# Kernel tuning notes

Hardware: AMD Instinct MI355X
Metric: run time of the kernel (lower is better)

The kernel has to match this reference:

```python
import jax, jax.numpy as jnp
import numpy as np

B, T, D_IN, H = 2048, 240, 180, 90


def setup_inputs() -> dict:
    key = jax.random.key(0)
    k1, k2, k3, k4, k5 = jax.random.split(key, 5)
    s = 1.0 / np.sqrt(H)  # torch LSTMCell init scale
    return {
        "x": jax.random.normal(k1, (B, 3, 60, 240), dtype=jnp.float32),
        "W_ih": jax.random.uniform(k2, (4 * H, D_IN), dtype=jnp.float32, minval=-s, maxval=s),
        "W_hh": jax.random.uniform(k3, (4 * H, H), dtype=jnp.float32, minval=-s, maxval=s),
        "b_ih": jax.random.uniform(k4, (4 * H,), dtype=jnp.float32, minval=-s, maxval=s),
        "b_hh": jax.random.uniform(k5, (4 * H,), dtype=jnp.float32, minval=-s, maxval=s),
    }


def reference(x, W_ih, W_hh, b_ih, b_hh):
    # (B, 3, 60, 240) -> (B, 240, 3, 60) -> (B, 240, 180)
    b = x.shape[0]
    xt = jnp.transpose(x, (0, 3, 1, 2)).reshape(b, T, D_IN)
    # NOTE: the torch module calls LSTMCell without carrying state, so h0=c0=0
    # at EVERY timestep; the W_hh contribution is identically zero and all
    # timesteps are independent -> one batched GEMM over (B*T).
    gates = jnp.einsum("bti,gi->btg", xt, W_ih) + b_ih + b_hh  # (B, T, 4H)
    i_g, f_g, g_g, o_g = jnp.split(gates, 4, axis=-1)  # torch gate order i,f,g,o
    c = jax.nn.sigmoid(i_g) * jnp.tanh(g_g)  # f_g * c_prev = 0
    h = jax.nn.sigmoid(o_g) * jnp.tanh(c)
    return jax.nn.sigmoid(h)  # (B, T, H)
```

## Files before the change

### kernel.cpp

```cpp
#include <hip/hip_runtime.h>


#define B_SZ 2048
#define T_SZ 240
#define K_SZ 180
#define H_SZ 90
#define KP   192
#define TB   80
#define NP   3
#define NTT  5

#define WS_B_OFF 110592

typedef __bf16 bf16x8 __attribute__((ext_vector_type(8)));
typedef __bf16 bf16x4 __attribute__((ext_vector_type(4)));
typedef float  f32x4  __attribute__((ext_vector_type(4)));

__device__ __forceinline__ float sigmoidf_(float x) {
    return __builtin_amdgcn_rcpf(1.0f + __expf(-x));
}
__device__ __forceinline__ float tanhf_(float x) {
    return 1.0f - 2.0f * __builtin_amdgcn_rcpf(__expf(2.0f * x) + 1.0f);
}

__device__ __forceinline__ int skey(int t) {
    return (2 * (t + (t >> 4))) & 14;
}
__device__ __forceinline__ int sgran(int g, int t) {
    return (g & ~15) | ((g ^ skey(t)) & 15);
}

__global__ __launch_bounds__(384) void prepack_kernel(
    const float* __restrict__ W_ih,
    const float* __restrict__ b_ih,
    const float* __restrict__ b_hh,
    void* __restrict__ ws)
{
    __bf16* wp = (__bf16*)ws;
    float*  bp = (float*)((char*)ws + WS_B_OFF);
    const int gb[3] = {0, 180, 270};

    const int bid = blockIdx.x;
    const int tid = threadIdx.x;
    if (bid < 18) {
        const int g  = bid / 6;
        const int ks = bid % 6;
        const int w  = tid >> 6;
        const int l  = tid & 63;
        const int q  = l >> 4;
        const int n  = l & 15;
        const int h  = w * 16 + n;
        bf16x8 f;
        #pragma unroll
        for (int j = 0; j < 8; ++j) {
            int k = ks * 32 + q * 8 + j;
            float v = (h < H_SZ && k < K_SZ) ? W_ih[(size_t)(gb[g] + h) * K_SZ + k] : 0.0f;
            f[j] = (__bf16)v;
        }
        *(bf16x8*)(wp + (size_t)(((g * 6 + ks) * 6 + w) * 64 + l) * 8) = f;
    } else {
        if (tid < 288) {
            int g = tid / 96, hh = tid % 96;
            bp[g * 96 + hh] = (hh < H_SZ) ? (b_ih[gb[g] + hh] + b_hh[gb[g] + hh]) : 0.0f;
        }
    }
}

__global__ __launch_bounds__(384, 3) void lstm_fused_kernel(
    const float* __restrict__ x,
    const void*  __restrict__ ws,
    float* __restrict__ out)
{
    __shared__ __align__(16) __bf16 aBuf[TB * KP];

    const int bid  = blockIdx.x;
    const int b    = bid / NP;
    const int part = bid - b * NP;
    const int t0   = part * TB;

    const int tid  = threadIdx.x;
    const int wave = tid >> 6;
    const int lane = tid & 63;
    const int q    = lane >> 4;
    const int n    = lane & 15;
    const int h    = wave * 16 + n;
    const bool hv  = (h < H_SZ);

    const float* xb = x + (size_t)b * (K_SZ * T_SZ) + t0;

    if (tid < TB * 3) {
        int t  = tid / 3;
        int gz = 45 + (tid - (tid / 3) * 3);
        *(unsigned long long*)(aBuf + t * KP + sgran(gz, t) * 4) = 0ull;
    }

    #pragma unroll
    for (int p = 0; p < 3; ++p) {
        int u = tid + p * 384;
        if (p < 2 || u < 900) {
            int k4 = u / 20;
            int t4 = u - k4 * 20;
            const float* src = xb + (k4 * 4) * T_SZ + t4 * 4;
            f32x4 r0 = *(const f32x4*)(src);
            f32x4 r1 = *(const f32x4*)(src + T_SZ);
            f32x4 r2 = *(const f32x4*)(src + 2 * T_SZ);
            f32x4 r3 = *(const f32x4*)(src + 3 * T_SZ);
            #pragma unroll
            for (int j = 0; j < 4; ++j) {
                int t = t4 * 4 + j;
                bf16x4 w;
                w[0] = (__bf16)r0[j]; w[1] = (__bf16)r1[j];
                w[2] = (__bf16)r2[j]; w[3] = (__bf16)r3[j];
                *(bf16x4*)(aBuf + t * KP + sgran(k4, t) * 4) = w;
            }
        }
    }

    const bf16x8* wp = (const bf16x8*)ws;
    bf16x8 bfrag[3][6];
    #pragma unroll
    for (int g = 0; g < 3; ++g)
        #pragma unroll
        for (int ks = 0; ks < 6; ++ks)
            bfrag[g][ks] = wp[((g * 6 + ks) * 6 + wave) * 64 + lane];

    const float* bp = (const float*)((const char*)ws + WS_B_OFF);
    const float bias_i = bp[0 * 96 + h];
    const float bias_g = bp[1 * 96 + h];
    const float bias_o = bp[2 * 96 + h];
    float* ob = out + (size_t)b * (T_SZ * H_SZ) + (size_t)t0 * H_SZ;

    __syncthreads();

    #pragma unroll
    for (int tt = 0; tt < NTT; ++tt) {
        f32x4 acc0 = {0.f, 0.f, 0.f, 0.f};
        f32x4 acc1 = {0.f, 0.f, 0.f, 0.f};
        f32x4 acc2 = {0.f, 0.f, 0.f, 0.f};
        const int t = tt * 16 + n;
        #pragma unroll
        for (int ks = 0; ks < 6; ++ks) {
            int g = ks * 8 + 2 * q;
            bf16x8 a = *(const bf16x8*)(aBuf + t * KP + sgran(g, t) * 4);
            acc0 = __builtin_amdgcn_mfma_f32_16x16x32_bf16(a, bfrag[0][ks], acc0, 0, 0, 0);
            acc1 = __builtin_amdgcn_mfma_f32_16x16x32_bf16(a, bfrag[1][ks], acc1, 0, 0, 0);
            acc2 = __builtin_amdgcn_mfma_f32_16x16x32_bf16(a, bfrag[2][ks], acc2, 0, 0, 0);
        }
        if (hv) {
            const int tg = tt * 16 + q * 4;
            #pragma unroll
            for (int e = 0; e < 4; ++e) {
                float gi = acc0[e] + bias_i;
                float gg = acc1[e] + bias_g;
                float go = acc2[e] + bias_o;
                float cc = sigmoidf_(gi) * tanhf_(gg);
                float hh = sigmoidf_(go) * tanhf_(cc);
                ob[(size_t)(tg + e) * H_SZ + h] = sigmoidf_(hh);
            }
        }
        if (tt + 1 < NTT) __builtin_amdgcn_s_barrier();
    }
}

extern "C" void kernel_launch(void* const* d_in, const int* in_sizes, int n_in,
                              void* d_out, int out_size, void* d_ws, size_t ws_size,
                              hipStream_t stream) {
    const float* x    = (const float*)d_in[0];
    const float* W_ih = (const float*)d_in[1];
    const float* b_ih = (const float*)d_in[3];
    const float* b_hh = (const float*)d_in[4];
    float* out = (float*)d_out;

    prepack_kernel<<<dim3(19), dim3(384), 0, stream>>>(W_ih, b_ih, b_hh, d_ws);
    lstm_fused_kernel<<<dim3(B_SZ * NP), dim3(384), 0, stream>>>(x, d_ws, out);
}
```

Baseline: 554.5 us.

## Make LSTM kernel persistent with double-buffered LDS prefetch of input tiles

Replaces the one-block-per-tile grid with 512 persistent blocks, each handling 12 consecutive (batch, time-part) tiles. The global loads for the next tile are issued into registers before the MFMA and epilogue work on the current tile, then written to a second LDS buffer, so load latency overlaps with compute. This also amortises the per-block weight-fragment and bias loads across tiles. In exchange it doubles LDS use, raises register pressure from the prefetch registers, and leaves fewer blocks in the grid, which may lower occupancy and load balance.

```diff
diff --git a/kernel.cpp b/kernel.cpp
--- a/kernel.cpp
+++ b/kernel.cpp
@@ -7,8 +7,10 @@
 #define H_SZ 90
 #define KP   192
 #define TB   80
-#define NP   3
 #define NTT  5
+#define BPB  4
+#define NPARTS 12
+#define NBLK 512
 
 #define WS_B_OFF 110592
 
@@ -71,12 +73,7 @@
     const void*  __restrict__ ws,
     float* __restrict__ out)
 {
-    __shared__ __align__(16) __bf16 aBuf[TB * KP];
-
-    const int bid  = blockIdx.x;
-    const int b    = bid / NP;
-    const int part = bid - b * NP;
-    const int t0   = part * TB;
+    __shared__ __align__(16) __bf16 aBuf[2][TB * KP];
 
     const int tid  = threadIdx.x;
     const int wave = tid >> 6;
@@ -86,36 +83,6 @@
     const int h    = wave * 16 + n;
     const bool hv  = (h < H_SZ);
 
-    const float* xb = x + (size_t)b * (K_SZ * T_SZ) + t0;
-
-    if (tid < TB * 3) {
-        int t  = tid / 3;
-        int gz = 45 + (tid - (tid / 3) * 3);
-        *(unsigned long long*)(aBuf + t * KP + sgran(gz, t) * 4) = 0ull;
-    }
-
-    #pragma unroll
-    for (int p = 0; p < 3; ++p) {
-        int u = tid + p * 384;
-        if (p < 2 || u < 900) {
-            int k4 = u / 20;
-            int t4 = u - k4 * 20;
-            const float* src = xb + (k4 * 4) * T_SZ + t4 * 4;
-            f32x4 r0 = *(const f32x4*)(src);
-            f32x4 r1 = *(const f32x4*)(src + T_SZ);
-            f32x4 r2 = *(const f32x4*)(src + 2 * T_SZ);
-            f32x4 r3 = *(const f32x4*)(src + 3 * T_SZ);
-            #pragma unroll
-            for (int j = 0; j < 4; ++j) {
-                int t = t4 * 4 + j;
-                bf16x4 w;
-                w[0] = (__bf16)r0[j]; w[1] = (__bf16)r1[j];
-                w[2] = (__bf16)r2[j]; w[3] = (__bf16)r3[j];
-                *(bf16x4*)(aBuf + t * KP + sgran(k4, t) * 4) = w;
-            }
-        }
-    }
-
     const bf16x8* wp = (const bf16x8*)ws;
     bf16x8 bfrag[3][6];
     #pragma unroll
@@ -128,38 +95,111 @@
     const float bias_i = bp[0 * 96 + h];
     const float bias_g = bp[1 * 96 + h];
     const float bias_o = bp[2 * 96 + h];
-    float* ob = out + (size_t)b * (T_SZ * H_SZ) + (size_t)t0 * H_SZ;
-
+
+    if (tid < TB * 3) {
+        int t  = tid / 3;
+        int gz = 45 + (tid - (tid / 3) * 3);
+        *(unsigned long long*)(aBuf[0] + t * KP + sgran(gz, t) * 4) = 0ull;
+        *(unsigned long long*)(aBuf[1] + t * KP + sgran(gz, t) * 4) = 0ull;
+    }
+
+    const int k4a = tid / 20,           t4a = tid - (tid / 20) * 20;
+    const int k4b = (tid + 384) / 20,   t4b = (tid + 384) - ((tid + 384) / 20) * 20;
+    const int k4c = (tid + 768) / 20,   t4c = (tid + 768) - ((tid + 768) / 20) * 20;
+    const bool u2v = (tid < 132);
+
+    const int b0 = blockIdx.x * BPB;
+
+#define LOADU(R, K4, T4, XB)                                            \
+    {                                                                   \
+        const float* src = (XB) + ((K4) * 4) * T_SZ + (T4) * 4;         \
+        R[0] = *(const f32x4*)(src);                                    \
+        R[1] = *(const f32x4*)(src + T_SZ);                             \
+        R[2] = *(const f32x4*)(src + 2 * T_SZ);                         \
+        R[3] = *(const f32x4*)(src + 3 * T_SZ);                         \
+    }
+#define WRITEU(DST, R, K4, T4)                                          \
+    {                                                                   \
+        _Pragma("unroll")                                               \
+        for (int j = 0; j < 4; ++j) {                                   \
+            int t = (T4) * 4 + j;                                       \
+            bf16x4 w;                                                   \
+            w[0] = (__bf16)R[0][j]; w[1] = (__bf16)R[1][j];             \
+            w[2] = (__bf16)R[2][j]; w[3] = (__bf16)R[3][j];             \
+            *(bf16x4*)((DST) + t * KP + sgran((K4), t) * 4) = w;        \
+        }                                                               \
+    }
+
+    f32x4 r0[4], r1[4], r2[4];
+
+    {
+        const float* xb = x + (size_t)b0 * (K_SZ * T_SZ);
+        LOADU(r0, k4a, t4a, xb);
+        LOADU(r1, k4b, t4b, xb);
+        if (u2v) LOADU(r2, k4c, t4c, xb);
+        WRITEU(aBuf[0], r0, k4a, t4a);
+        WRITEU(aBuf[0], r1, k4b, t4b);
+        if (u2v) WRITEU(aBuf[0], r2, k4c, t4c);
+    }
     __syncthreads();
 
-    #pragma unroll
-    for (int tt = 0; tt < NTT; ++tt) {
-        f32x4 acc0 = {0.f, 0.f, 0.f, 0.f};
-        f32x4 acc1 = {0.f, 0.f, 0.f, 0.f};
-        f32x4 acc2 = {0.f, 0.f, 0.f, 0.f};
-        const int t = tt * 16 + n;
+    int bb = b0, pp = 0;
+    #pragma unroll 1
+    for (int gp = 0; gp < NPARTS; ++gp) {
+        const int cur = gp & 1;
+
+        int bn = bb, pn = pp + 1;
+        if (pn == 3) { pn = 0; ++bn; }
+        if (gp + 1 < NPARTS) {
+            const float* xb = x + (size_t)bn * (K_SZ * T_SZ) + pn * TB;
+            LOADU(r0, k4a, t4a, xb);
+            LOADU(r1, k4b, t4b, xb);
+            if (u2v) LOADU(r2, k4c, t4c, xb);
+        }
+
+        const __bf16* ab = aBuf[cur];
+        float* ob = out + (size_t)bb * (T_SZ * H_SZ) + (size_t)(pp * TB) * H_SZ;
         #pragma unroll
-        for (int ks = 0; ks < 6; ++ks) {
-            int g = ks * 8 + 2 * q;
-            bf16x8 a = *(const bf16x8*)(aBuf + t * KP + sgran(g, t) * 4);
-            acc0 = __builtin_amdgcn_mfma_f32_16x16x32_bf16(a, bfrag[0][ks], acc0, 0, 0, 0);
-            acc1 = __builtin_amdgcn_mfma_f32_16x16x32_bf16(a, bfrag[1][ks], acc1, 0, 0, 0);
-            acc2 = __builtin_amdgcn_mfma_f32_16x16x32_bf16(a, bfrag[2][ks], acc2, 0, 0, 0);
-        }
-        if (hv) {
-            const int tg = tt * 16 + q * 4;
+        for (int tt = 0; tt < NTT; ++tt) {
+            f32x4 acc0 = {0.f, 0.f, 0.f, 0.f};
+            f32x4 acc1 = {0.f, 0.f, 0.f, 0.f};
+            f32x4 acc2 = {0.f, 0.f, 0.f, 0.f};
+            const int t = tt * 16 + n;
             #pragma unroll
-            for (int e = 0; e < 4; ++e) {
-                float gi = acc0[e] + bias_i;
-                float gg = acc1[e] + bias_g;
-                float go = acc2[e] + bias_o;
-                float cc = sigmoidf_(gi) * tanhf_(gg);
-                float hh = sigmoidf_(go) * tanhf_(cc);
-                ob[(size_t)(tg + e) * H_SZ + h] = sigmoidf_(hh);
+            for (int ks = 0; ks < 6; ++ks) {
+                int g = ks * 8 + 2 * q;
+                bf16x8 a = *(const bf16x8*)(ab + t * KP + sgran(g, t) * 4);
+                acc0 = __builtin_amdgcn_mfma_f32_16x16x32_bf16(a, bfrag[0][ks], acc0, 0, 0, 0);
+                acc1 = __builtin_amdgcn_mfma_f32_16x16x32_bf16(a, bfrag[1][ks], acc1, 0, 0, 0);
+                acc2 = __builtin_amdgcn_mfma_f32_16x16x32_bf16(a, bfrag[2][ks], acc2, 0, 0, 0);
             }
-        }
-        if (tt + 1 < NTT) __builtin_amdgcn_s_barrier();
-    }
+            if (hv) {
+                const int tg = tt * 16 + q * 4;
+                #pragma unroll
+                for (int e = 0; e < 4; ++e) {
+                    float gi = acc0[e] + bias_i;
+                    float gg = acc1[e] + bias_g;
+                    float go = acc2[e] + bias_o;
+                    float cc = sigmoidf_(gi) * tanhf_(gg);
+                    float hh = sigmoidf_(go) * tanhf_(cc);
+                    ob[(size_t)(tg + e) * H_SZ + h] = sigmoidf_(hh);
+                }
+            }
+            if (tt + 1 < NTT) __builtin_amdgcn_s_barrier();
+        }
+
+        if (gp + 1 < NPARTS) {
+            __bf16* dst = aBuf[cur ^ 1];
+            WRITEU(dst, r0, k4a, t4a);
+            WRITEU(dst, r1, k4b, t4b);
+            if (u2v) WRITEU(dst, r2, k4c, t4c);
+        }
+        __syncthreads();
+        bb = bn; pp = pn;
+    }
+
+#undef LOADU
+#undef WRITEU
 }
 
 extern "C" void kernel_launch(void* const* d_in, const int* in_sizes, int n_in,
@@ -172,5 +212,5 @@
     float* out = (float*)d_out;
 
     prepack_kernel<<<dim3(19), dim3(384), 0, stream>>>(W_ih, b_ih, b_hh, d_ws);
-    lstm_fused_kernel<<<dim3(B_SZ * NP), dim3(384), 0, stream>>>(x, d_ws, out);
-}
+    lstm_fused_kernel<<<dim3(NBLK), dim3(384), 0, stream>>>(x, d_ws, out);
+}
```

Result: slower. 692.2 us (+24.8%).

## Split x staging into two phases overlapping second load with first tiles' compute

Applied to the files above, without the earlier changes.

Stages only the first 48 timesteps of the x tile into LDS before the first barrier, computes three 16-row tiles, then stages the remaining 32 timesteps and computes the last two tiles. The goal is to start MFMA work sooner and overlap part of the global load with compute, shortening the serial load-then-compute prologue. It adds an extra __syncthreads, and the second-phase loads are issued after compute rather than prefetched early, so their latency may simply be exposed later in the block.

```diff
diff --git a/kernel.cpp b/kernel.cpp
--- a/kernel.cpp
+++ b/kernel.cpp
@@ -94,26 +94,32 @@
         *(unsigned long long*)(aBuf + t * KP + sgran(gz, t) * 4) = 0ull;
     }
 
-    #pragma unroll
-    for (int p = 0; p < 3; ++p) {
-        int u = tid + p * 384;
-        if (p < 2 || u < 900) {
-            int k4 = u / 20;
-            int t4 = u - k4 * 20;
-            const float* src = xb + (k4 * 4) * T_SZ + t4 * 4;
-            f32x4 r0 = *(const f32x4*)(src);
-            f32x4 r1 = *(const f32x4*)(src + T_SZ);
-            f32x4 r2 = *(const f32x4*)(src + 2 * T_SZ);
-            f32x4 r3 = *(const f32x4*)(src + 3 * T_SZ);
-            #pragma unroll
-            for (int j = 0; j < 4; ++j) {
-                int t = t4 * 4 + j;
-                bf16x4 w;
-                w[0] = (__bf16)r0[j]; w[1] = (__bf16)r1[j];
-                w[2] = (__bf16)r2[j]; w[3] = (__bf16)r3[j];
-                *(bf16x4*)(aBuf + t * KP + sgran(k4, t) * 4) = w;
-            }
-        }
+#define STAGE_UNIT(K4, TBASE)                                           \
+    {                                                                   \
+        const float* src = xb + ((K4) * 4) * T_SZ + (TBASE);            \
+        f32x4 r0 = *(const f32x4*)(src);                                \
+        f32x4 r1 = *(const f32x4*)(src + T_SZ);                         \
+        f32x4 r2 = *(const f32x4*)(src + 2 * T_SZ);                     \
+        f32x4 r3 = *(const f32x4*)(src + 3 * T_SZ);                     \
+        _Pragma("unroll")                                               \
+        for (int j = 0; j < 4; ++j) {                                   \
+            int t = (TBASE) + j;                                        \
+            bf16x4 w;                                                   \
+            w[0] = (__bf16)r0[j]; w[1] = (__bf16)r1[j];                 \
+            w[2] = (__bf16)r2[j]; w[3] = (__bf16)r3[j];                 \
+            *(bf16x4*)(aBuf + t * KP + sgran((K4), t) * 4) = w;         \
+        }                                                               \
+    }
+
+    {
+        int u  = tid;
+        int k4 = u / 12, t4 = u - (u / 12) * 12;
+        STAGE_UNIT(k4, t4 * 4);
+    }
+    if (tid < 156) {
+        int u  = tid + 384;
+        int k4 = u / 12, t4 = u - (u / 12) * 12;
+        STAGE_UNIT(k4, t4 * 4);
     }
 
     const bf16x8* wp = (const bf16x8*)ws;
@@ -132,34 +138,51 @@
 
     __syncthreads();
 
-    #pragma unroll
-    for (int tt = 0; tt < NTT; ++tt) {
-        f32x4 acc0 = {0.f, 0.f, 0.f, 0.f};
-        f32x4 acc1 = {0.f, 0.f, 0.f, 0.f};
-        f32x4 acc2 = {0.f, 0.f, 0.f, 0.f};
-        const int t = tt * 16 + n;
-        #pragma unroll
-        for (int ks = 0; ks < 6; ++ks) {
-            int g = ks * 8 + 2 * q;
-            bf16x8 a = *(const bf16x8*)(aBuf + t * KP + sgran(g, t) * 4);
-            acc0 = __builtin_amdgcn_mfma_f32_16x16x32_bf16(a, bfrag[0][ks], acc0, 0, 0, 0);
-            acc1 = __builtin_amdgcn_mfma_f32_16x16x32_bf16(a, bfrag[1][ks], acc1, 0, 0, 0);
-            acc2 = __builtin_amdgcn_mfma_f32_16x16x32_bf16(a, bfrag[2][ks], acc2, 0, 0, 0);
-        }
-        if (hv) {
-            const int tg = tt * 16 + q * 4;
-            #pragma unroll
-            for (int e = 0; e < 4; ++e) {
-                float gi = acc0[e] + bias_i;
-                float gg = acc1[e] + bias_g;
-                float go = acc2[e] + bias_o;
-                float cc = sigmoidf_(gi) * tanhf_(gg);
-                float hh = sigmoidf_(go) * tanhf_(cc);
-                ob[(size_t)(tg + e) * H_SZ + h] = sigmoidf_(hh);
-            }
-        }
-        if (tt + 1 < NTT) __builtin_amdgcn_s_barrier();
+#define COMPUTE_TILE(TT)                                                \
+    {                                                                   \
+        f32x4 acc0 = {0.f, 0.f, 0.f, 0.f};                              \
+        f32x4 acc1 = {0.f, 0.f, 0.f, 0.f};                              \
+        f32x4 acc2 = {0.f, 0.f, 0.f, 0.f};                              \
+        const int t = (TT) * 16 + n;                                    \
+        _Pragma("unroll")                                               \
+        for (int ks = 0; ks < 6; ++ks) {                                \
+            int g = ks * 8 + 2 * q;                                     \
+            bf16x8 a = *(const bf16x8*)(aBuf + t * KP + sgran(g, t) * 4); \
+            acc0 = __builtin_amdgcn_mfma_f32_16x16x32_bf16(a, bfrag[0][ks], acc0, 0, 0, 0); \
+            acc1 = __builtin_amdgcn_mfma_f32_16x16x32_bf16(a, bfrag[1][ks], acc1, 0, 0, 0); \
+            acc2 = __builtin_amdgcn_mfma_f32_16x16x32_bf16(a, bfrag[2][ks], acc2, 0, 0, 0); \
+        }                                                               \
+        if (hv) {                                                       \
+            const int tg = (TT) * 16 + q * 4;                           \
+            _Pragma("unroll")                                           \
+            for (int e = 0; e < 4; ++e) {                               \
+                float gi = acc0[e] + bias_i;                            \
+                float gg = acc1[e] + bias_g;                            \
+                float go = acc2[e] + bias_o;                            \
+                float cc = sigmoidf_(gi) * tanhf_(gg);                  \
+                float hh = sigmoidf_(go) * tanhf_(cc);                  \
+                ob[(size_t)(tg + e) * H_SZ + h] = sigmoidf_(hh);        \
+            }                                                           \
+        }                                                               \
     }
+
+    COMPUTE_TILE(0)
+    COMPUTE_TILE(1)
+    COMPUTE_TILE(2)
+
+    if (tid < 360) {
+        int u  = tid;
+        int k4 = u / 8, t4 = u - (u / 8) * 8;
+        STAGE_UNIT(k4, 48 + t4 * 4);
+    }
+    __syncthreads();
+
+    COMPUTE_TILE(3)
+    __builtin_amdgcn_s_barrier();
+    COMPUTE_TILE(4)
+
+#undef STAGE_UNIT
+#undef COMPUTE_TILE
 }
 
 extern "C" void kernel_launch(void* const* d_in, const int* in_sizes, int n_in,
```

Result: slower. 567.4 us (+2.3%).
